# Kernel tuning notes

Measured on AMD Instinct MI355X. Metric: run time of the kernel, lower is better.

## Reference

```python
import jax, jax.numpy as jnp
import numpy as np

N_NODES = 80000
N_EDGES = 1280000
IN_C, HID_C, OUT_C = 128, 64, 40


def setup_inputs() -> dict:
    key = jax.random.key(0)
    k1, k2, k3, k4 = jax.random.split(key, 4)
    x = jax.random.normal(k1, (N_NODES, IN_C), dtype=jnp.float32)
    edge_index = jax.random.randint(k2, (2, N_EDGES), 0, N_NODES, dtype=jnp.int32)
    W1 = jax.random.normal(k3, (IN_C, HID_C), dtype=jnp.float32) * (1.0 / np.sqrt(IN_C))
    W2 = jax.random.normal(k4, (HID_C, OUT_C), dtype=jnp.float32) * (1.0 / np.sqrt(HID_C))
    return {"x": x, "edge_index": edge_index, "W1": W1, "W2": W2}


def _spmm_add(edge_index, h):
    # adj_t.matmul(h): out[dst] += h[src]  (aggr='add', message = x_j)
    src, dst = edge_index[0], edge_index[1]
    return jax.ops.segment_sum(h[src], dst, num_segments=N_NODES)


def reference(x, edge_index, W1, W2):
    # GCNConv 1: linear (no bias) then add-aggregate SpMM
    h = _spmm_add(edge_index, x @ W1)          # [N, HID]
    h = jax.nn.relu(h)
    # GCNConv 2
    h = _spmm_add(edge_index, h @ W2)          # [N, OUT]
    return jax.nn.log_softmax(h, axis=-1)
```

## Files before the change

### kernel.cpp

```cpp
#include <hip/hip_runtime.h>
#include <hip/hip_bf16.h>
#include <math.h>

#define N_NODES 80000
#define N_EDGES 1280000
#define IN_C 128
#define HID_C 64
#define OUT_C 40

#define KB 313
#define BK_CAP 4600
#define EPT_A 8

__device__ __forceinline__ float bf_lo(unsigned u) {
    union { unsigned i; float f; } c; c.i = u << 16; return c.f;
}
__device__ __forceinline__ float bf_hi(unsigned u) {
    union { unsigned i; float f; } c; c.i = u & 0xffff0000u; return c.f;
}
__device__ __forceinline__ unsigned pack_bf2(float a, float b) {
    union { float f; unsigned i; } ca, cb; ca.f = a; cb.f = b;
    unsigned ra = (ca.i + 0x7fffu + ((ca.i >> 16) & 1u)) >> 16;
    unsigned rb = (cb.i + 0x7fffu + ((cb.i >> 16) & 1u)) >> 16;
    return ra | (rb << 16);
}

typedef short v8s __attribute__((ext_vector_type(8)));
typedef float v4f __attribute__((ext_vector_type(4)));
typedef float v2f __attribute__((ext_vector_type(2)));
union U16 { uint4 u; v8s s; };

__device__ __forceinline__ v2f bf2f(unsigned u) {
    return (v2f){bf_lo(u), bf_hi(u)};
}

__global__ void prep_w_kernel(const float* __restrict__ W1, const float* __restrict__ W2,
                              unsigned* __restrict__ w1t, unsigned* __restrict__ w2t,
                              int* __restrict__ bcnt) {
    const int g = blockIdx.x * 256 + threadIdx.x;
    if (g < KB) bcnt[g] = 0;
    {
        const int wcol = g >> 6, kk = g & 63;
        w1t[g] = pack_bf2(W1[(2 * kk) * HID_C + wcol], W1[(2 * kk + 1) * HID_C + wcol]);
    }
    if (g < 1536) {
        const int wcol = g >> 5, kk = g & 31;
        w2t[g] = (wcol < OUT_C)
            ? pack_bf2(W2[(2 * kk) * OUT_C + wcol], W2[(2 * kk + 1) * OUT_C + wcol])
            : 0u;
    }
}

__global__ __launch_bounds__(512) void binA_kernel(const int* __restrict__ src,
                                                   const int* __restrict__ dst,
                                                   int* __restrict__ bcnt,
                                                   int* __restrict__ gbuf) {
    __shared__ int lcnt[KB];
    __shared__ int lexcl[KB];
    __shared__ int lbase[KB];
    __shared__ int lcur[KB];
    __shared__ int stage[512 * EPT_A];
    __shared__ int gaddr[512 * EPT_A];
    const int tid = threadIdx.x;

    for (int i = tid; i < KB; i += 512) lcnt[i] = 0;
    __syncthreads();

    const int e0 = blockIdx.x * 512 * EPT_A;
    int my_s[EPT_A], my_b[EPT_A], my_dl[EPT_A];
#pragma unroll
    for (int j = 0; j < EPT_A; ++j) {
        const int e = e0 + j * 512 + tid;
        if (e < N_EDGES) {
            const int d = dst[e];
            my_s[j] = src[e];
            my_b[j] = d >> 8;
            my_dl[j] = d & 255;
            atomicAdd(&lcnt[my_b[j]], 1);
        } else my_b[j] = -1;
    }
    __syncthreads();

    if (tid < KB) lexcl[tid] = lcnt[tid];
    __syncthreads();
    for (int o = 1; o < KB; o <<= 1) {
        int t = (tid < KB && tid >= o) ? lexcl[tid - o] : 0;
        __syncthreads();
        if (tid < KB) lexcl[tid] += t;
        __syncthreads();
    }
    const int total = lexcl[KB - 1];
    if (tid < KB) {
        lexcl[tid] -= lcnt[tid];
        lbase[tid] = (lcnt[tid] > 0) ? atomicAdd(&bcnt[tid], lcnt[tid]) : 0;
        lcur[tid] = 0;
    }
    __syncthreads();

#pragma unroll
    for (int j = 0; j < EPT_A; ++j) {
        if (my_b[j] >= 0) {
            const int b = my_b[j];
            const int r = atomicAdd(&lcur[b], 1);
            const int li = lexcl[b] + r;
            stage[li] = (my_s[j] << 8) | my_dl[j];
            int gp = lbase[b] + r;
            if (gp >= BK_CAP) gp = BK_CAP - 1;
            gaddr[li] = b * BK_CAP + gp;
        }
    }
    __syncthreads();

    for (int i = tid; i < total; i += 512)
        gbuf[gaddr[i]] = stage[i];
}

__global__ __launch_bounds__(512) void binB_kernel(const int* __restrict__ bcnt,
                                                   const int* __restrict__ gbuf,
                                                   int* __restrict__ rp,
                                                   int* __restrict__ col) {
    __shared__ int sc[KB];
    __shared__ int hist[256];
    __shared__ int excl[256];
    __shared__ int cur[256];
    __shared__ int outb[BK_CAP];
    const int b = blockIdx.x;
    const int tid = threadIdx.x;

    if (tid < KB) sc[tid] = min(bcnt[tid], BK_CAP);
    __syncthreads();
    for (int o = 1; o < KB; o <<= 1) {
        int t = (tid < KB && tid >= o) ? sc[tid - o] : 0;
        __syncthreads();
        if (tid < KB) sc[tid] += t;
        __syncthreads();
    }
    const int n = min(bcnt[b], BK_CAP);
    const int cbase = sc[b] - n;
    const int* __restrict__ my = gbuf + (size_t)b * BK_CAP;

    if (tid < 256) hist[tid] = 0;
    __syncthreads();
    for (int i = tid; i < n; i += 512)
        atomicAdd(&hist[my[i] & 255], 1);
    __syncthreads();

    int h = 0;
    if (tid < 256) { h = hist[tid]; excl[tid] = h; }
    __syncthreads();
    for (int o = 1; o < 256; o <<= 1) {
        int t = (tid < 256 && tid >= o) ? excl[tid - o] : 0;
        __syncthreads();
        if (tid < 256) excl[tid] += t;
        __syncthreads();
    }
    if (tid < 256) {
        const int ex = excl[tid] - h;
        cur[tid] = ex;
        const int node = b * 256 + tid;
        if (node <= N_NODES) rp[node] = cbase + ex;
    }
    __syncthreads();

    for (int i = tid; i < n; i += 512) {
        const int pk = my[i];
        const int pos = atomicAdd(&cur[pk & 255], 1);
        outb[pos] = pk >> 8;
    }
    __syncthreads();
    for (int i = tid; i < n; i += 512)
        col[cbase + i] = outb[i];
}

__global__ __launch_bounds__(256) void gemm1_kernel(const float* __restrict__ x,
                                                    const unsigned* __restrict__ w1t,
                                                    unsigned* __restrict__ h1b) {
    const int wave = threadIdx.x >> 6, lane = threadIdx.x & 63;
    const int nl = lane & 15, quad = lane >> 4;
    const int node = (blockIdx.x * 4 + wave) * 16 + nl;

    v4f acc[4];
#pragma unroll
    for (int q = 0; q < 4; ++q) acc[q] = (v4f){0.f, 0.f, 0.f, 0.f};

#pragma unroll
    for (int kit = 0; kit < 4; ++kit) {
        const float* xp = x + (size_t)node * IN_C + kit * 32 + quad * 8;
        const float4 lo = *(const float4*)xp;
        const float4 hi = *(const float4*)(xp + 4);
        U16 bu;
        bu.u.x = pack_bf2(lo.x, lo.y); bu.u.y = pack_bf2(lo.z, lo.w);
        bu.u.z = pack_bf2(hi.x, hi.y); bu.u.w = pack_bf2(hi.z, hi.w);
#pragma unroll
        for (int mt = 0; mt < 4; ++mt) {
            U16 au;
            au.u = *(const uint4*)(w1t + ((mt * 16 + nl) * 64 + kit * 16 + quad * 4));
            acc[mt] = __builtin_amdgcn_mfma_f32_16x16x32_bf16(au.s, bu.s, acc[mt], 0, 0, 0);
        }
    }
#pragma unroll
    for (int mt = 0; mt < 4; ++mt) {
        uint2 o;
        o.x = pack_bf2(acc[mt][0], acc[mt][1]);
        o.y = pack_bf2(acc[mt][2], acc[mt][3]);
        *(uint2*)(h1b + (size_t)node * 32 + mt * 8 + quad * 2) = o;
    }
}

__global__ void gather64_kernel(const int* __restrict__ rp, const int* __restrict__ col,
                                const unsigned* __restrict__ h1b,
                                unsigned* __restrict__ agg1b) {
    __shared__ int lcol[768];
    const int tid = threadIdx.x;
    const int lane = tid & 63;
    const int wave = tid >> 6;
    const int sl = lane & 31;
    const int es = sl >> 3;
    const int cl = sl & 7;
    const int nb = blockIdx.x * 8;

    const int seg_b = rp[nb];
    const int seg_n = min(rp[nb + 8] - seg_b, 768);
    for (int i = tid; i < seg_n; i += 256) lcol[i] = col[seg_b + i];
    __syncthreads();

    const int node = nb + wave * 2 + (lane >> 5);
    const int b = rp[node], e = rp[node + 1];

    v2f acc[4];
#pragma unroll
    for (int k = 0; k < 4; ++k) acc[k] = (v2f){0.f, 0.f};

    for (int pos = b; __any(pos < e); pos += 32) {
#pragma unroll
        for (int j = 0; j < 8; ++j) {
            const int ei = pos + (j << 2) + es;
            if (ei < e) {
                const int o = ei - seg_b;
                const int s = (o < seg_n) ? lcol[o] : col[ei];
                const uint4 v = *(const uint4*)(h1b + (size_t)s * 32 + cl * 4);
                acc[0] += bf2f(v.x); acc[1] += bf2f(v.y);
                acc[2] += bf2f(v.z); acc[3] += bf2f(v.w);
            }
        }
    }
#pragma unroll
    for (int k = 0; k < 4; ++k) {
        acc[k][0] += __shfl_down(acc[k][0], 16, 64);
        acc[k][1] += __shfl_down(acc[k][1], 16, 64);
    }
#pragma unroll
    for (int k = 0; k < 4; ++k) {
        acc[k][0] += __shfl_down(acc[k][0], 8, 64);
        acc[k][1] += __shfl_down(acc[k][1], 8, 64);
    }

    if (sl < 8) {
        uint4 o;
        o.x = pack_bf2(fmaxf(acc[0][0], 0.f), fmaxf(acc[0][1], 0.f));
        o.y = pack_bf2(fmaxf(acc[1][0], 0.f), fmaxf(acc[1][1], 0.f));
        o.z = pack_bf2(fmaxf(acc[2][0], 0.f), fmaxf(acc[2][1], 0.f));
        o.w = pack_bf2(fmaxf(acc[3][0], 0.f), fmaxf(acc[3][1], 0.f));
        *(uint4*)(agg1b + (size_t)node * 32 + cl * 4) = o;
    }
}

__global__ __launch_bounds__(256) void gemm2_kernel(const unsigned* __restrict__ agg1b,
                                                    const unsigned* __restrict__ w2t,
                                                    unsigned* __restrict__ h2f) {
    const int wave = threadIdx.x >> 6, lane = threadIdx.x & 63;
    const int nl = lane & 15, quad = lane >> 4;
    const int node = (blockIdx.x * 4 + wave) * 16 + nl;

    v4f c[3];
#pragma unroll
    for (int q = 0; q < 3; ++q) c[q] = (v4f){0.f, 0.f, 0.f, 0.f};

#pragma unroll
    for (int kit = 0; kit < 2; ++kit) {
        U16 bu;
        bu.u = *(const uint4*)(agg1b + (size_t)node * 32 + kit * 16 + quad * 4);
#pragma unroll
        for (int mt = 0; mt < 3; ++mt) {
            U16 au;
            au.u = *(const uint4*)(w2t + ((mt * 16 + nl) * 32 + kit * 16 + quad * 4));
            c[mt] = __builtin_amdgcn_mfma_f32_16x16x32_bf16(au.s, bu.s, c[mt], 0, 0, 0);
        }
    }
#pragma unroll
    for (int mt = 0; mt < 3; ++mt) {
        const int idx = mt * 4 + quad;
        if (idx < 10) {
            int u = 0;
            u = __builtin_amdgcn_cvt_pk_fp8_f32(c[mt][0], c[mt][1], u, false);
            u = __builtin_amdgcn_cvt_pk_fp8_f32(c[mt][2], c[mt][3], u, true);
            h2f[(size_t)node * 10 + idx] = (unsigned)u;
        }
    }
}

__global__ void gather40_ls_kernel(const int* __restrict__ rp, const int* __restrict__ col,
                                   const unsigned* __restrict__ h2f,
                                   float* __restrict__ out) {
    __shared__ int lcol[1024];
    const int tid = threadIdx.x;
    const int lane = tid & 63;
    const int wave = tid >> 6;
    const int sl = lane & 15;
    const int es = sl / 5;
    const int cl = sl - es * 5;
    const int gbase = lane & 48;
    const int nb = blockIdx.x * 16;

    const int seg_b = rp[nb];
    const int seg_n = min(rp[nb + 16] - seg_b, 1024);
    for (int i = tid; i < seg_n; i += 256) lcol[i] = col[seg_b + i];
    __syncthreads();

    const int node = nb + wave * 4 + (lane >> 4);
    const int b = rp[node], e = rp[node + 1];

    v2f a[4];
#pragma unroll
    for (int k = 0; k < 4; ++k) a[k] = (v2f){0.f, 0.f};

    for (int pos = b; __any(pos < e); pos += 24) {
#pragma unroll
        for (int j = 0; j < 8; ++j) {
            const int ei = pos + j * 3 + es;
            if ((es < 3) && (ei < e)) {
                const int o = ei - seg_b;
                const int s = (o < seg_n) ? lcol[o] : col[ei];
                const uint2 v = *(const uint2*)(h2f + (size_t)s * 10 + cl * 2);
                a[0] += __builtin_amdgcn_cvt_pk_f32_fp8((int)v.x, false);
                a[1] += __builtin_amdgcn_cvt_pk_f32_fp8((int)v.x, true);
                a[2] += __builtin_amdgcn_cvt_pk_f32_fp8((int)v.y, false);
                a[3] += __builtin_amdgcn_cvt_pk_f32_fp8((int)v.y, true);
            }
        }
    }
#pragma unroll
    for (int k = 0; k < 4; ++k) {
#pragma unroll
        for (int h = 0; h < 2; ++h) {
            const float u = __shfl_down(a[k][h], 5, 64);
            const float w = __shfl_down(a[k][h], 10, 64);
            a[k][h] += u + w;
        }
    }

    const bool own = sl < 5;
    float m = -INFINITY;
    if (own) {
#pragma unroll
        for (int k = 0; k < 4; ++k) m = fmaxf(m, fmaxf(a[k][0], a[k][1]));
    }
    const float m0 = __shfl(m, gbase + 0, 64), m1 = __shfl(m, gbase + 1, 64);
    const float m2 = __shfl(m, gbase + 2, 64), m3 = __shfl(m, gbase + 3, 64);
    const float m4 = __shfl(m, gbase + 4, 64);
    const float gm = fmaxf(fmaxf(fmaxf(m0, m1), fmaxf(m2, m3)), m4);

    float s = 0.f;
    if (own) {
#pragma unroll
        for (int k = 0; k < 4; ++k)
            s += __expf(a[k][0] - gm) + __expf(a[k][1] - gm);
    }
    const float s0 = __shfl(s, gbase + 0, 64), s1 = __shfl(s, gbase + 1, 64);
    const float s2 = __shfl(s, gbase + 2, 64), s3 = __shfl(s, gbase + 3, 64);
    const float s4 = __shfl(s, gbase + 4, 64);
    const float ls = __logf(s0 + s1 + s2 + s3 + s4) + gm;

    if (own) {
        float* op = out + (size_t)node * OUT_C + cl * 8;
        *(float4*)op = make_float4(a[0][0] - ls, a[0][1] - ls, a[1][0] - ls, a[1][1] - ls);
        *(float4*)(op + 4) = make_float4(a[2][0] - ls, a[2][1] - ls, a[3][0] - ls, a[3][1] - ls);
    }
}

extern "C" void kernel_launch(void* const* d_in, const int* in_sizes, int n_in,
                              void* d_out, int out_size, void* d_ws, size_t ws_size,
                              hipStream_t stream) {
    const float* x  = (const float*)d_in[0];
    const int* eidx = (const int*)d_in[1];
    const float* W1 = (const float*)d_in[2];
    const float* W2 = (const float*)d_in[3];
    float* out = (float*)d_out;

    const int* src = eidx;
    const int* dst = eidx + N_EDGES;

    unsigned* h1b   = (unsigned*)d_ws;
    unsigned* agg1b = h1b + (size_t)N_NODES * 32;
    unsigned* h2f   = agg1b + (size_t)N_NODES * 32;
    int*      gbuf  = (int*)(h2f + (size_t)N_NODES * 10);
    int*      col   = gbuf + (size_t)KB * BK_CAP;
    int*      rp    = col + N_EDGES;
    int*      bcnt  = rp + (N_NODES + 1);
    unsigned* w1t   = (unsigned*)(bcnt + KB);
    unsigned* w2t   = w1t + 4096;

    prep_w_kernel<<<16, 256, 0, stream>>>(W1, W2, w1t, w2t, bcnt);
    binA_kernel<<<(N_EDGES + 512 * EPT_A - 1) / (512 * EPT_A), 512, 0, stream>>>(src, dst, bcnt, gbuf);
    binB_kernel<<<KB, 512, 0, stream>>>(bcnt, gbuf, rp, col);
    gemm1_kernel<<<N_NODES / 64, 256, 0, stream>>>(x, w1t, h1b);

    gather64_kernel<<<N_NODES / 8, 256, 0, stream>>>(rp, col, h1b, agg1b);
    gemm2_kernel<<<N_NODES / 64, 256, 0, stream>>>(agg1b, w2t, h2f);
    gather40_ls_kernel<<<N_NODES / 16, 256, 0, stream>>>(rp, col, h2f, out);
}
```

Before: 181.9 us.

## Fuse CSR bucket sort, layer-1 gather and GEMM2 into one kernel

After: 185.7 us. 2.1% more time.

```diff
diff --git a/kernel.cpp b/kernel.cpp
--- a/kernel.cpp
+++ b/kernel.cpp
@@ -8,9 +8,9 @@
 #define HID_C 64
 #define OUT_C 40
 
-#define KB 313
-#define BK_CAP 4600
-#define EPT_A 8
+#define KB 625
+#define BK_CAP 2400
+#define NPAIR 313
 
 __device__ __forceinline__ float bf_lo(unsigned u) {
     union { unsigned i; float f; } c; c.i = u << 16; return c.f;
@@ -59,117 +59,59 @@
     __shared__ int lexcl[KB];
     __shared__ int lbase[KB];
     __shared__ int lcur[KB];
-    __shared__ int stage[512 * EPT_A];
-    __shared__ int gaddr[512 * EPT_A];
+    __shared__ int pp[NPAIR];
+    __shared__ int stage[2048];
+    __shared__ int gaddr[2048];
     const int tid = threadIdx.x;
 
     for (int i = tid; i < KB; i += 512) lcnt[i] = 0;
     __syncthreads();
 
-    const int e0 = blockIdx.x * 512 * EPT_A;
-    int my_s[EPT_A], my_b[EPT_A], my_dl[EPT_A];
-#pragma unroll
-    for (int j = 0; j < EPT_A; ++j) {
+    const int e0 = blockIdx.x * 2048;
+    int my_s[4], my_b[4], my_dl[4];
+#pragma unroll
+    for (int j = 0; j < 4; ++j) {
         const int e = e0 + j * 512 + tid;
-        if (e < N_EDGES) {
-            const int d = dst[e];
-            my_s[j] = src[e];
-            my_b[j] = d >> 8;
-            my_dl[j] = d & 255;
-            atomicAdd(&lcnt[my_b[j]], 1);
-        } else my_b[j] = -1;
-    }
-    __syncthreads();
-
-    if (tid < KB) lexcl[tid] = lcnt[tid];
-    __syncthreads();
-    for (int o = 1; o < KB; o <<= 1) {
-        int t = (tid < KB && tid >= o) ? lexcl[tid - o] : 0;
-        __syncthreads();
-        if (tid < KB) lexcl[tid] += t;
-        __syncthreads();
-    }
-    const int total = lexcl[KB - 1];
-    if (tid < KB) {
-        lexcl[tid] -= lcnt[tid];
-        lbase[tid] = (lcnt[tid] > 0) ? atomicAdd(&bcnt[tid], lcnt[tid]) : 0;
-        lcur[tid] = 0;
-    }
-    __syncthreads();
-
-#pragma unroll
-    for (int j = 0; j < EPT_A; ++j) {
-        if (my_b[j] >= 0) {
-            const int b = my_b[j];
-            const int r = atomicAdd(&lcur[b], 1);
-            const int li = lexcl[b] + r;
-            stage[li] = (my_s[j] << 8) | my_dl[j];
-            int gp = lbase[b] + r;
-            if (gp >= BK_CAP) gp = BK_CAP - 1;
-            gaddr[li] = b * BK_CAP + gp;
-        }
+        const int d = dst[e];
+        my_s[j] = src[e];
+        my_b[j] = d >> 7;
+        my_dl[j] = d & 127;
+        atomicAdd(&lcnt[my_b[j]], 1);
+    }
+    __syncthreads();
+
+    if (tid < NPAIR) pp[tid] = lcnt[2 * tid] + ((2 * tid + 1 < KB) ? lcnt[2 * tid + 1] : 0);
+    __syncthreads();
+    for (int o = 1; o < NPAIR; o <<= 1) {
+        int t = (tid < NPAIR && tid >= o) ? pp[tid - o] : 0;
+        __syncthreads();
+        if (tid < NPAIR) pp[tid] += t;
+        __syncthreads();
+    }
+    const int total = pp[NPAIR - 1];
+    for (int i = tid; i < KB; i += 512) {
+        const int half = i >> 1;
+        const int ex = (half > 0 ? pp[half - 1] : 0) + ((i & 1) ? lcnt[i - 1] : 0);
+        lexcl[i] = ex;
+        lbase[i] = (lcnt[i] > 0) ? atomicAdd(&bcnt[i], lcnt[i]) : 0;
+        lcur[i] = 0;
+    }
+    __syncthreads();
+
+#pragma unroll
+    for (int j = 0; j < 4; ++j) {
+        const int b = my_b[j];
+        const int r = atomicAdd(&lcur[b], 1);
+        const int li = lexcl[b] + r;
+        stage[li] = (my_s[j] << 7) | my_dl[j];
+        int gp = lbase[b] + r;
+        if (gp >= BK_CAP) gp = BK_CAP - 1;
+        gaddr[li] = b * BK_CAP + gp;
     }
     __syncthreads();
 
     for (int i = tid; i < total; i += 512)
         gbuf[gaddr[i]] = stage[i];
-}
-
-__global__ __launch_bounds__(512) void binB_kernel(const int* __restrict__ bcnt,
-                                                   const int* __restrict__ gbuf,
-                                                   int* __restrict__ rp,
-                                                   int* __restrict__ col) {
-    __shared__ int sc[KB];
-    __shared__ int hist[256];
-    __shared__ int excl[256];
-    __shared__ int cur[256];
-    __shared__ int outb[BK_CAP];
-    const int b = blockIdx.x;
-    const int tid = threadIdx.x;
-
-    if (tid < KB) sc[tid] = min(bcnt[tid], BK_CAP);
-    __syncthreads();
-    for (int o = 1; o < KB; o <<= 1) {
-        int t = (tid < KB && tid >= o) ? sc[tid - o] : 0;
-        __syncthreads();
-        if (tid < KB) sc[tid] += t;
-        __syncthreads();
-    }
-    const int n = min(bcnt[b], BK_CAP);
-    const int cbase = sc[b] - n;
-    const int* __restrict__ my = gbuf + (size_t)b * BK_CAP;
-
-    if (tid < 256) hist[tid] = 0;
-    __syncthreads();
-    for (int i = tid; i < n; i += 512)
-        atomicAdd(&hist[my[i] & 255], 1);
-    __syncthreads();
-
-    int h = 0;
-    if (tid < 256) { h = hist[tid]; excl[tid] = h; }
-    __syncthreads();
-    for (int o = 1; o < 256; o <<= 1) {
-        int t = (tid < 256 && tid >= o) ? excl[tid - o] : 0;
-        __syncthreads();
-        if (tid < 256) excl[tid] += t;
-        __syncthreads();
-    }
-    if (tid < 256) {
-        const int ex = excl[tid] - h;
-        cur[tid] = ex;
-        const int node = b * 256 + tid;
-        if (node <= N_NODES) rp[node] = cbase + ex;
-    }
-    __syncthreads();
-
-    for (int i = tid; i < n; i += 512) {
-        const int pk = my[i];
-        const int pos = atomicAdd(&cur[pk & 255], 1);
-        outb[pos] = pk >> 8;
-    }
-    __syncthreads();
-    for (int i = tid; i < n; i += 512)
-        col[cbase + i] = outb[i];
 }
 
 __global__ __launch_bounds__(256) void gemm1_kernel(const float* __restrict__ x,
@@ -207,70 +149,113 @@
     }
 }
 
-__global__ void gather64_kernel(const int* __restrict__ rp, const int* __restrict__ col,
-                                const unsigned* __restrict__ h1b,
-                                unsigned* __restrict__ agg1b) {
-    __shared__ int lcol[768];
+__global__ __launch_bounds__(512) void binB_g64_gemm2_kernel(
+        const int* __restrict__ bcnt, const int* __restrict__ gbuf,
+        int* __restrict__ rp, int* __restrict__ col,
+        const unsigned* __restrict__ h1b, const unsigned* __restrict__ w2t,
+        unsigned* __restrict__ h2f) {
+    __shared__ int sc[KB];
+    __shared__ int pp[NPAIR];
+    __shared__ int hist[128];
+    __shared__ int excl[128];
+    __shared__ int cur[128];
+    __shared__ int outb[BK_CAP];
+    __shared__ unsigned aggs[128 * 36];
+    const int b = blockIdx.x;
     const int tid = threadIdx.x;
-    const int lane = tid & 63;
-    const int wave = tid >> 6;
-    const int sl = lane & 31;
-    const int es = sl >> 3;
-    const int cl = sl & 7;
-    const int nb = blockIdx.x * 8;
-
-    const int seg_b = rp[nb];
-    const int seg_n = min(rp[nb + 8] - seg_b, 768);
-    for (int i = tid; i < seg_n; i += 256) lcol[i] = col[seg_b + i];
-    __syncthreads();
-
-    const int node = nb + wave * 2 + (lane >> 5);
-    const int b = rp[node], e = rp[node + 1];
-
-    v2f acc[4];
-#pragma unroll
-    for (int k = 0; k < 4; ++k) acc[k] = (v2f){0.f, 0.f};
-
-    for (int pos = b; __any(pos < e); pos += 32) {
-#pragma unroll
-        for (int j = 0; j < 8; ++j) {
-            const int ei = pos + (j << 2) + es;
-            if (ei < e) {
-                const int o = ei - seg_b;
-                const int s = (o < seg_n) ? lcol[o] : col[ei];
-                const uint4 v = *(const uint4*)(h1b + (size_t)s * 32 + cl * 4);
-                acc[0] += bf2f(v.x); acc[1] += bf2f(v.y);
-                acc[2] += bf2f(v.z); acc[3] += bf2f(v.w);
+
+    for (int i = tid; i < KB; i += 512) sc[i] = min(bcnt[i], BK_CAP);
+    __syncthreads();
+    if (tid < NPAIR) pp[tid] = sc[2 * tid] + ((2 * tid + 1 < KB) ? sc[2 * tid + 1] : 0);
+    __syncthreads();
+    for (int o = 1; o < NPAIR; o <<= 1) {
+        int t = (tid < NPAIR && tid >= o) ? pp[tid - o] : 0;
+        __syncthreads();
+        if (tid < NPAIR) pp[tid] += t;
+        __syncthreads();
+    }
+    const int n = sc[b];
+    const int half = b >> 1;
+    const int cbase = (half > 0 ? pp[half - 1] : 0) + ((b & 1) ? sc[b - 1] : 0);
+    const int* __restrict__ my = gbuf + (size_t)b * BK_CAP;
+
+    if (tid < 128) hist[tid] = 0;
+    __syncthreads();
+    for (int i = tid; i < n; i += 512)
+        atomicAdd(&hist[my[i] & 127], 1);
+    __syncthreads();
+    if (tid < 128) excl[tid] = hist[tid];
+    __syncthreads();
+    for (int o = 1; o < 128; o <<= 1) {
+        int t = (tid < 128 && tid >= o) ? excl[tid - o] : 0;
+        __syncthreads();
+        if (tid < 128) excl[tid] += t;
+        __syncthreads();
+    }
+    if (tid < 128) {
+        const int ex = excl[tid] - hist[tid];
+        cur[tid] = ex;
+        rp[b * 128 + tid] = cbase + ex;
+        excl[tid] = ex;
+    }
+    if (b == KB - 1 && tid == 128) rp[N_NODES] = cbase + n;
+    __syncthreads();
+
+    for (int i = tid; i < n; i += 512) {
+        const int pk = my[i];
+        const int pos = atomicAdd(&cur[pk & 127], 1);
+        outb[pos] = pk >> 7;
+    }
+    __syncthreads();
+    for (int i = tid; i < n; i += 512)
+        col[cbase + i] = outb[i];
+
+    const int lane = tid & 63, wave = tid >> 6;
+    const int sl = lane & 31, es = sl >> 3, cl = sl & 7;
+    for (int pass = 0; pass < 8; ++pass) {
+        const int nl = pass * 16 + wave * 2 + (lane >> 5);
+        const int lb = excl[nl];
+        const int le = lb + hist[nl];
+
+        v2f acc[4];
+#pragma unroll
+        for (int k = 0; k < 4; ++k) acc[k] = (v2f){0.f, 0.f};
+
+        for (int pos = lb; __any(pos < le); pos += 32) {
+#pragma unroll
+            for (int j = 0; j < 8; ++j) {
+                const int ei = pos + (j << 2) + es;
+                if (ei < le) {
+                    const int s = outb[ei];
+                    const uint4 v = *(const uint4*)(h1b + (size_t)s * 32 + cl * 4);
+                    acc[0] += bf2f(v.x); acc[1] += bf2f(v.y);
+                    acc[2] += bf2f(v.z); acc[3] += bf2f(v.w);
+                }
             }
         }
-    }
-#pragma unroll
-    for (int k = 0; k < 4; ++k) {
-        acc[k][0] += __shfl_down(acc[k][0], 16, 64);
-        acc[k][1] += __shfl_down(acc[k][1], 16, 64);
-    }
-#pragma unroll
-    for (int k = 0; k < 4; ++k) {
-        acc[k][0] += __shfl_down(acc[k][0], 8, 64);
-        acc[k][1] += __shfl_down(acc[k][1], 8, 64);
-    }
-
-    if (sl < 8) {
-        uint4 o;
-        o.x = pack_bf2(fmaxf(acc[0][0], 0.f), fmaxf(acc[0][1], 0.f));
-        o.y = pack_bf2(fmaxf(acc[1][0], 0.f), fmaxf(acc[1][1], 0.f));
-        o.z = pack_bf2(fmaxf(acc[2][0], 0.f), fmaxf(acc[2][1], 0.f));
-        o.w = pack_bf2(fmaxf(acc[3][0], 0.f), fmaxf(acc[3][1], 0.f));
-        *(uint4*)(agg1b + (size_t)node * 32 + cl * 4) = o;
-    }
-}
-
-__global__ __launch_bounds__(256) void gemm2_kernel(const unsigned* __restrict__ agg1b,
-                                                    const unsigned* __restrict__ w2t,
-                                                    unsigned* __restrict__ h2f) {
-    const int wave = threadIdx.x >> 6, lane = threadIdx.x & 63;
-    const int nl = lane & 15, quad = lane >> 4;
-    const int node = (blockIdx.x * 4 + wave) * 16 + nl;
+#pragma unroll
+        for (int k = 0; k < 4; ++k) {
+            acc[k][0] += __shfl_down(acc[k][0], 16, 64);
+            acc[k][1] += __shfl_down(acc[k][1], 16, 64);
+        }
+#pragma unroll
+        for (int k = 0; k < 4; ++k) {
+            acc[k][0] += __shfl_down(acc[k][0], 8, 64);
+            acc[k][1] += __shfl_down(acc[k][1], 8, 64);
+        }
+        if (sl < 8) {
+            uint4 o;
+            o.x = pack_bf2(fmaxf(acc[0][0], 0.f), fmaxf(acc[0][1], 0.f));
+            o.y = pack_bf2(fmaxf(acc[1][0], 0.f), fmaxf(acc[1][1], 0.f));
+            o.z = pack_bf2(fmaxf(acc[2][0], 0.f), fmaxf(acc[2][1], 0.f));
+            o.w = pack_bf2(fmaxf(acc[3][0], 0.f), fmaxf(acc[3][1], 0.f));
+            *(uint4*)&aggs[nl * 36 + cl * 4] = o;
+        }
+    }
+    __syncthreads();
+
+    const int nl16 = lane & 15, quad = lane >> 4;
+    const int node = b * 128 + wave * 16 + nl16;
 
     v4f c[3];
 #pragma unroll
@@ -279,11 +264,11 @@
 #pragma unroll
     for (int kit = 0; kit < 2; ++kit) {
         U16 bu;
-        bu.u = *(const uint4*)(agg1b + (size_t)node * 32 + kit * 16 + quad * 4);
+        bu.u = *(const uint4*)&aggs[(wave * 16 + nl16) * 36 + kit * 16 + quad * 4];
 #pragma unroll
         for (int mt = 0; mt < 3; ++mt) {
             U16 au;
-            au.u = *(const uint4*)(w2t + ((mt * 16 + nl) * 32 + kit * 16 + quad * 4));
+            au.u = *(const uint4*)(w2t + ((mt * 16 + nl16) * 32 + kit * 16 + quad * 4));
             c[mt] = __builtin_amdgcn_mfma_f32_16x16x32_bf16(au.s, bu.s, c[mt], 0, 0, 0);
         }
     }
@@ -391,8 +376,7 @@
     const int* dst = eidx + N_EDGES;
 
     unsigned* h1b   = (unsigned*)d_ws;
-    unsigned* agg1b = h1b + (size_t)N_NODES * 32;
-    unsigned* h2f   = agg1b + (size_t)N_NODES * 32;
+    unsigned* h2f   = h1b + (size_t)N_NODES * 32;
     int*      gbuf  = (int*)(h2f + (size_t)N_NODES * 10);
     int*      col   = gbuf + (size_t)KB * BK_CAP;
     int*      rp    = col + N_EDGES;
@@ -401,11 +385,8 @@
     unsigned* w2t   = w1t + 4096;
 
     prep_w_kernel<<<16, 256, 0, stream>>>(W1, W2, w1t, w2t, bcnt);
-    binA_kernel<<<(N_EDGES + 512 * EPT_A - 1) / (512 * EPT_A), 512, 0, stream>>>(src, dst, bcnt, gbuf);
-    binB_kernel<<<KB, 512, 0, stream>>>(bcnt, gbuf, rp, col);
+    binA_kernel<<<KB, 512, 0, stream>>>(src, dst, bcnt, gbuf);
     gemm1_kernel<<<N_NODES / 64, 256, 0, stream>>>(x, w1t, h1b);
-
-    gather64_kernel<<<N_NODES / 8, 256, 0, stream>>>(rp, col, h1b, agg1b);
-    gemm2_kernel<<<N_NODES / 64, 256, 0, stream>>>(agg1b, w2t, h2f);
+    binB_g64_gemm2_kernel<<<KB, 512, 0, stream>>>(bcnt, gbuf, rp, col, h1b, w2t, h2f);
     gather40_ls_kernel<<<N_NODES / 16, 256, 0, stream>>>(rp, col, h2f, out);
 }
```
